# Kernel tuning notes

Hardware: AMD Instinct MI355X
Metric: run time of the kernel (lower is better)

Reference implementation:

```python
import jax, jax.numpy as jnp
from jax import lax
import numpy as np

NF, G, K = 64, 8, 3
B, H, W = 4, 128, 128
KK = K * K
CG = NF // G  # channels per deformable group


def setup_inputs() -> dict:
    key = jax.random.key(0)
    ks = jax.random.split(key, 8)
    f32 = jnp.float32
    s = 0.05  # small init so predicted offsets stay in a realistic range
    return {
        'nbr_fea_l': jax.random.normal(ks[0], (B, NF, H, W), f32),
        'ref_fea_l': jax.random.normal(ks[1], (B, NF, H, W), f32),
        'w_off1': jax.random.normal(ks[2], (NF, 2 * NF, K, K), f32) * s,
        'b_off1': jax.random.normal(ks[3], (NF,), f32) * s,
        'w_om': jax.random.normal(ks[4], (3 * G * KK, NF, K, K), f32) * s,
        'b_om': jax.random.normal(ks[5], (3 * G * KK,), f32) * s,
        'w_dcn': jax.random.normal(ks[6], (NF, NF, K, K), f32) * s,
        'b_dcn': jax.random.normal(ks[7], (NF,), f32) * s,
    }


def _conv3(x, w, b):
    # 3x3, stride 1, pad 1, NCHW/OIHW
    y = lax.conv_general_dilated(x, w, (1, 1), ((1, 1), (1, 1)))
    return y + b[None, :, None, None]


def _lrelu(x):
    return jnp.where(x >= 0, x, 0.1 * x)


def _gather_one(xf, idx):
    # xf: [CG, H*W], idx: [KK, H, W] -> [CG, KK, H, W]
    return jnp.take(xf, idx, axis=1)


_gather = jax.vmap(jax.vmap(_gather_one))  # over B, G


def _bilinear(x_flat, py, px):
    # x_flat: [B,G,CG,H*W]; py/px: [B,G,KK,H,W] sample coords
    y0f = jnp.floor(py)
    x0f = jnp.floor(px)
    wy = py - y0f
    wx = px - x0f
    y0 = y0f.astype(jnp.int32)
    x0 = x0f.astype(jnp.int32)
    out = jnp.zeros(x_flat.shape[:3] + py.shape[2:], x_flat.dtype)
    corners = [(0, 0, (1 - wy) * (1 - wx)), (0, 1, (1 - wy) * wx),
               (1, 0, wy * (1 - wx)), (1, 1, wy * wx)]
    for dy, dx, wgt in corners:
        yy = y0 + dy
        xx = x0 + dx
        valid = ((yy >= 0) & (yy < H) & (xx >= 0) & (xx < W)).astype(x_flat.dtype)
        idx = jnp.clip(yy, 0, H - 1) * W + jnp.clip(xx, 0, W - 1)
        g = _gather(x_flat, idx)  # [B,G,CG,KK,H,W]
        out = out + g * (wgt * valid)[:, :, None]
    return out


def _forward(nbr, ref, w_off1, b_off1, w_om, b_om, w_dcn, b_dcn):
    # offset feature branch
    off_feat = _lrelu(_conv3(jnp.concatenate([nbr, ref], axis=1), w_off1, b_off1))
    om = _conv3(off_feat, w_om, b_om)  # [B, 3*G*KK, H, W]
    o1, o2, m = jnp.split(om, 3, axis=1)
    off_y = o1.reshape(B, G, KK, H, W)
    off_x = o2.reshape(B, G, KK, H, W)
    mask = jax.nn.sigmoid(m).reshape(B, G, KK, H, W)
    # kernel tap displacements (pad=1, dilation=1, stride=1)
    dy = (jnp.repeat(jnp.arange(K), K) - 1).astype(nbr.dtype)  # [KK]
    dx = (jnp.tile(jnp.arange(K), K) - 1).astype(nbr.dtype)
    hh = jnp.arange(H, dtype=nbr.dtype)
    ww = jnp.arange(W, dtype=nbr.dtype)
    py = hh[None, None, None, :, None] + dy[None, None, :, None, None] + off_y
    px = ww[None, None, None, None, :] + dx[None, None, :, None, None] + off_x
    x_flat = nbr.reshape(B, G, CG, H * W)
    sampled = _bilinear(x_flat, py, px)           # [B,G,CG,KK,H,W]
    sampled = sampled * mask[:, :, None]          # modulated (DCNv2)
    w = w_dcn.reshape(NF, G, CG, KK)
    out = jnp.einsum('bgckhw,ogck->bohw', sampled, w) + b_dcn[None, :, None, None]
    return _lrelu(out)


def reference(nbr_fea_l, ref_fea_l, w_off1, b_off1, w_om, b_om, w_dcn, b_dcn):
    return _forward(nbr_fea_l, ref_fea_l, w_off1, b_off1, w_om, b_om, w_dcn, b_dcn)
```

## Files before the change

kernel.cpp:

```cpp
#include <hip/hip_runtime.h>
#include <hip/hip_bf16.h>
#include <hip/hip_fp16.h>
#include <cmath>

#define NF 64
#define GRP 8
#define CG 8
#define KK 9
#define HH 128
#define WWID 128
#define BB 4
#define HWSZ (HH * WWID)
#define C_OM 216
#define OMS 292
#define DPS 72

typedef __attribute__((ext_vector_type(8))) short bf16x8;
typedef __attribute__((ext_vector_type(8))) _Float16 f16x8;
typedef __attribute__((ext_vector_type(4))) float f32x4;

__device__ inline unsigned short f2bf(float f) {
    union { float f; unsigned u; } x; x.f = f;
    unsigned r = x.u + 0x7fff + ((x.u >> 16) & 1);
    return (unsigned short)(r >> 16);
}

__global__ __launch_bounds__(256) void prep_kernel(
    const float* __restrict__ nbr, const float* __restrict__ ref,
    const float* __restrict__ w1, const float* __restrict__ wom,
    const float* __restrict__ wdcn,
    unsigned short* __restrict__ out, unsigned short* __restrict__ gm,
    unsigned short* __restrict__ wf1, unsigned short* __restrict__ wf2,
    unsigned short* __restrict__ wdf)
{
    __shared__ unsigned short lds[64 * 136];
    __shared__ __half lds_h[64 * 72];
    const int tid = threadIdx.x;

    if (blockIdx.x < 1024) {
        const int blk = blockIdx.x;
        const int b = blk >> 8, rem = blk & 255, y = rem >> 1, x0 = (rem & 1) * 64;
        const size_t rowoff = (size_t)y * WWID + x0;

#pragma unroll
        for (int it = 0; it < 8; ++it) {
            int idx = it * 256 + tid;
            int c = idx >> 4, p4 = idx & 15;
            const float* src = (c < NF) ? (nbr + (size_t)(b * NF + c) * HWSZ)
                                        : (ref + (size_t)(b * NF + c - NF) * HWSZ);
            const float4 v = *(const float4*)(src + rowoff + p4 * 4);
            const float vv[4] = {v.x, v.y, v.z, v.w};
#pragma unroll
            for (int k = 0; k < 4; ++k) {
                const int p = p4 * 4 + k;
                lds[p * 136 + c] = f2bf(vv[k]);
                if (c < 64) lds_h[p * 72 + c] = __float2half(vv[k]);
            }
        }
        __syncthreads();
        const int p = tid >> 2, c0 = (tid & 3) * 32;
        unsigned short* dst = out + ((size_t)b * HWSZ + rowoff + p) * 128 + c0;
#pragma unroll
        for (int i = 0; i < 8; ++i)
            *(int2*)(dst + i * 4) = *(const int2*)&lds[p * 136 + c0 + i * 4];
        if (c0 < 64) {
#pragma unroll
            for (int gi = 0; gi < 4; ++gi) {
                const int g = (c0 >> 3) + gi;
                *(int4*)(gm + (((size_t)(b * 8 + g)) * HWSZ + rowoff + p) * 8) =
                    *(const int4*)&lds_h[p * 72 + g * 8];
            }
        }
        return;
    }

    int idx = (blockIdx.x - 1024) * 256 + tid;
    if (idx < 73728) {
        int j = idx & 7, lane = (idx >> 3) & 63, t = idx >> 9;
        int mt = t % 4, kt = t / 4;
        int c0 = (kt / 9) * 32, tap = kt - (kt / 9) * 9;
        int cout = mt * 16 + (lane & 15);
        int cin = c0 + ((lane >> 4) * 8) + j;
        wf1[idx] = f2bf(w1[((size_t)cout * 128 + cin) * KK + tap]);
        return;
    }
    idx -= 73728;
    if (idx < 129024) {
        int j = idx & 7, lane = (idx >> 3) & 63, t = idx >> 9;
        int mt = t % 14, kt = t / 14;
        int c0 = (kt / 9) * 32, tap = kt - (kt / 9) * 9;
        int cout = mt * 16 + (lane & 15);
        int cin = c0 + ((lane >> 4) * 8) + j;
        float v = (cout < C_OM) ? wom[((size_t)cout * 64 + cin) * KK + tap] : 0.f;
        wf2[idx] = f2bf(v);
        return;
    }
    idx -= 129024;
    if (idx < 36864) {
        int j = idx & 7, lane = (idx >> 3) & 63, t = idx >> 9;
        int mt = t & 3, s = t >> 2;
        int cout = mt * 16 + (lane & 15);
        int kglob = s * 32 + (lane >> 4) * 8 + j;
        int gk = kglob >> 3, c = kglob & 7;
        int g = gk / 9, kt = gk - g * 9;
        const __half hv = __float2half(wdcn[((size_t)cout * NF + g * 8 + c) * 9 + kt]);
        wdf[idx] = *(const unsigned short*)&hv;
    }
}

__global__ __launch_bounds__(256) void conv1_kernel(
    const unsigned short* __restrict__ in,
    const unsigned short* __restrict__ wf,
    const float* __restrict__ bias,
    unsigned short* __restrict__ dst)
{
    __shared__ unsigned short st[3 * 66 * DPS];

    const int tid = threadIdx.x;
    const int lane = tid & 63;
    const int wv = tid >> 6;
    const int ng = blockIdx.x;
    const int b = ng >> 8, rem = ng & 255;
    const int y = rem >> 1, x0 = (rem & 1) * 64;
    const int ln = lane & 15, kb = lane >> 4;

    f32x4 acc[4];
#pragma unroll
    for (int nt = 0; nt < 4; ++nt) acc[nt] = f32x4{0.f, 0.f, 0.f, 0.f};

    for (int ch0 = 0; ch0 < 128; ch0 += 64) {
        __syncthreads();
        for (int i = tid; i < 3 * 66 * 8; i += 256) {
            const int j = i & 7, t = i >> 3;
            const int px = t % 66, r = t / 66;
            const int yy = y + r - 1, xx = x0 + px - 1;
            int4 v = {0, 0, 0, 0};
            if ((unsigned)yy < (unsigned)HH && (unsigned)xx < (unsigned)WWID)
                v = *(const int4*)(in + ((size_t)b * HWSZ + yy * WWID + xx) * 128
                                      + ch0 + j * 8);
            *(int4*)&st[(r * 66 + px) * DPS + j * 8] = v;
        }
        __syncthreads();

        const int base_kt = (ch0 / 32) * 9;
        bf16x8 afA, afB;
        afA = *(const bf16x8*)(wf + (((size_t)base_kt * 4 + wv) * 64 + lane) * 8);

#pragma unroll
        for (int step = 0; step < 18; ++step) {
            const int cc = (step / 9) * 32;
            const int tap = step % 9;
            const int ky = tap / 3, kx = tap % 3;

            if (step < 17) {
                const int kt1 = base_kt + step + 1;
                bf16x8* alt = (step & 1) ? &afA : &afB;
                *alt = *(const bf16x8*)(wf + (((size_t)kt1 * 4 + wv) * 64 + lane) * 8);
            }

            bf16x8 bfrag[4];
#pragma unroll
            for (int nt = 0; nt < 4; ++nt) {
                const int px = nt * 16 + ln + kx;
                bfrag[nt] = *(const bf16x8*)&st[(ky * 66 + px) * DPS + cc + kb * 8];
            }

            const bf16x8 cur = (step & 1) ? afB : afA;
#pragma unroll
            for (int nt = 0; nt < 4; ++nt)
                acc[nt] = __builtin_amdgcn_mfma_f32_16x16x32_bf16(
                    cur, bfrag[nt], acc[nt], 0, 0, 0);
        }
    }

    const int cout = wv * 16 + kb * 4;
    const float b0 = bias[cout], b1 = bias[cout + 1];
    const float b2 = bias[cout + 2], b3 = bias[cout + 3];
#pragma unroll
    for (int nt = 0; nt < 4; ++nt) {
        const int px = x0 + nt * 16 + ln;
        const size_t pix = (size_t)b * HWSZ + (size_t)y * WWID + px;
        f32x4 v = acc[nt];
        v[0] += b0; v[1] += b1; v[2] += b2; v[3] += b3;
#pragma unroll
        for (int r = 0; r < 4; ++r) v[r] = (v[r] >= 0.f) ? v[r] : 0.1f * v[r];
        int2 pk;
        pk.x = (int)f2bf(v[0]) | ((int)f2bf(v[1]) << 16);
        pk.y = (int)f2bf(v[2]) | ((int)f2bf(v[3]) << 16);
        *(int2*)(dst + pix * 64 + cout) = pk;
    }
}

__global__ __launch_bounds__(512, 4) void dcn_fused_kernel(
    const unsigned short* __restrict__ off_f,
    const unsigned short* __restrict__ gm,
    const unsigned short* __restrict__ wf2,
    const float* __restrict__ bom,
    const unsigned short* __restrict__ wdf,
    const float* __restrict__ bdcn,
    float* __restrict__ out)
{
    __shared__ unsigned short smem[128 * OMS];

    const int raw = blockIdx.x;
    const int bid = (raw & 7) * 64 + (raw >> 3);
    const int b = bid >> 7;
    const int y = bid & 127;

    const int tid = threadIdx.x;
    const int lane = tid & 63;
    const int wv = tid >> 6;
    const int ln = lane & 15, kb = lane >> 4;

    for (int i = tid; i < 3 * 130 * 8; i += 512) {
        const int j = i & 7, t = i >> 3;
        const int px = t % 130, r = t / 130;
        const int yy = y + r - 1, xx = px - 1;
        int4 v = {0, 0, 0, 0};
        if ((unsigned)yy < (unsigned)HH && (unsigned)xx < (unsigned)WWID)
            v = *(const int4*)(off_f + ((size_t)b * HWSZ + yy * WWID + xx) * 64 + j * 8);
        *(int4*)&smem[(r * 130 + px) * DPS + j * 8] = v;
    }
    __syncthreads();

    f32x4 acc1[2][8];
#pragma unroll
    for (int i = 0; i < 2; ++i)
#pragma unroll
        for (int j = 0; j < 8; ++j) acc1[i][j] = f32x4{0.f, 0.f, 0.f, 0.f};

    {
        bf16x8 afA[2], afB[2];
#pragma unroll
        for (int i = 0; i < 2; ++i) {
            const int mt = wv + 8 * i;
            afA[i] = (mt < 14)
                ? ((const bf16x8*)wf2)[(size_t)mt * 64 + lane]
                : bf16x8{};
        }

#pragma unroll
        for (int step = 0; step < 18; ++step) {
            const int cc = (step / 9) * 32;
            const int tap = step % 9;
            const int ky = tap / 3, kx = tap % 3;

            if (step < 17) {
                const int kt1 = step + 1;
                bf16x8* alt = (step & 1) ? afA : afB;
#pragma unroll
                for (int i = 0; i < 2; ++i) {
                    const int mt = wv + 8 * i;
                    alt[i] = (mt < 14)
                        ? ((const bf16x8*)wf2)[(size_t)kt1 * 14 * 64 + (size_t)mt * 64 + lane]
                        : bf16x8{};
                }
            }

            bf16x8 bfrag[8];
#pragma unroll
            for (int nt = 0; nt < 8; ++nt) {
                const int px = nt * 16 + ln + kx;
                bfrag[nt] = *(const bf16x8*)&smem[(ky * 130 + px) * DPS + cc + kb * 8];
            }

            const bf16x8* cur = (step & 1) ? afB : afA;
#pragma unroll
            for (int i = 0; i < 2; ++i) {
                const int mt = wv + 8 * i;
                if (mt < 14) {
#pragma unroll
                    for (int nt = 0; nt < 8; ++nt)
                        acc1[i][nt] = __builtin_amdgcn_mfma_f32_16x16x32_bf16(
                            cur[i], bfrag[nt], acc1[i][nt], 0, 0, 0);
                }
            }
        }
    }
    __syncthreads();

    __half* smh = (__half*)smem;
#pragma unroll
    for (int i = 0; i < 2; ++i) {
        const int mt = wv + 8 * i;
        if (mt >= 14) continue;
        const int cb = mt * 16 + kb * 4;
#pragma unroll
        for (int nt = 0; nt < 8; ++nt) {
            const int px = nt * 16 + ln;
#pragma unroll
            for (int r = 0; r < 4; ++r) {
                const int c = cb + r;
                if (c < C_OM) {
                    const int field = (c >= 144) ? 2 : ((c >= 72) ? 1 : 0);
                    const int gk = c - field * 72;
                    float v = acc1[i][nt][r] + bom[c];
                    if (field == 2) v = 1.f / (1.f + __expf(-v));
                    smh[px * OMS + gk * 4 + field] = __float2half(v);
                }
            }
        }
    }
    __syncthreads();

    const int pxl = wv * 16 + ln;
    const int x = pxl;

    f32x4 acc[4];
#pragma unroll
    for (int mt = 0; mt < 4; ++mt) acc[mt] = f32x4{0.f, 0.f, 0.f, 0.f};

    const unsigned short* gmb = gm + (size_t)b * 8 * HWSZ * 8;

#pragma unroll
    for (int ch = 0; ch < 3; ++ch) {
        short4 q[6];
#pragma unroll
        for (int i = 0; i < 6; ++i) {
            const int gk = (ch * 6 + i) * 4 + kb;
            q[i] = *(const short4*)&smh[pxl * OMS + gk * 4];
        }

#pragma unroll
        for (int i = 0; i < 6; ++i) {
            const int s = ch * 6 + i;
            const int gk = s * 4 + kb;
            const int g = gk / 9;
            const int kt = gk - g * 9;

            const float oy = __half2float(((const __half*)&q[i])[0]);
            const float ox = __half2float(((const __half*)&q[i])[1]);
            const float mv = __half2float(((const __half*)&q[i])[2]);

            const float pyf = (float)(y + kt / 3 - 1) + oy;
            const float pxf = (float)(x + kt % 3 - 1) + ox;
            const float fy = floorf(pyf), fx = floorf(pxf);
            const float wy = pyf - fy, wx = pxf - fx;
            const int iy = (int)fy, ix = (int)fx;

            float w00 = (1.f - wy) * (1.f - wx);
            float w01 = (1.f - wy) * wx;
            float w10 = wy * (1.f - wx);
            float w11 = wy * wx;

            const bool vy0 = (iy >= 0) && (iy < HH);
            const bool vy1 = (iy + 1 >= 0) && (iy + 1 < HH);
            const bool vx0 = (ix >= 0) && (ix < WWID);
            const bool vx1 = (ix + 1 >= 0) && (ix + 1 < WWID);
            w00 *= (vy0 && vx0) ? mv : 0.f;
            w01 *= (vy0 && vx1) ? mv : 0.f;
            w10 *= (vy1 && vx0) ? mv : 0.f;
            w11 *= (vy1 && vx1) ? mv : 0.f;

            const int y0c = min(max(iy, 0), HH - 1);
            const int y1c = min(max(iy + 1, 0), HH - 1);
            const int x0c = min(max(ix, 0), WWID - 1);
            const int x1c = min(max(ix + 1, 0), WWID - 1);
            const int sel = x1c - x0c;

            const float wl0 = w00 + (sel ? 0.f : w01);
            const float wh0 = sel ? w01 : 0.f;
            const float wl1 = w10 + (sel ? 0.f : w11);
            const float wh1 = sel ? w11 : 0.f;

            const unsigned short* pgm = gmb + (size_t)g * HWSZ * 8;
            const size_t rec0 = (size_t)(y0c * WWID + x0c) * 8;
            const size_t rec1 = (size_t)(y1c * WWID + x0c) * 8;
            int4 L0 = *(const int4*)(pgm + rec0);
            int4 H0 = *(const int4*)(pgm + rec0 + 8);
            int4 L1 = *(const int4*)(pgm + rec1);
            int4 H1 = *(const int4*)(pgm + rec1 + 8);

            const __half2 wl0h = __float2half2_rn(wl0);
            const __half2 wh0h = __float2half2_rn(wh0);
            const __half2 wl1h = __float2half2_rn(wl1);
            const __half2 wh1h = __float2half2_rn(wh1);
            const __half2* l0 = (const __half2*)&L0;
            const __half2* h0 = (const __half2*)&H0;
            const __half2* l1 = (const __half2*)&L1;
            const __half2* h1 = (const __half2*)&H1;
            __half2 bp0 = __hfma2(l0[0], wl0h, __hfma2(h0[0], wh0h,
                          __hfma2(l1[0], wl1h, __hmul2(h1[0], wh1h))));
            __half2 bp1 = __hfma2(l0[1], wl0h, __hfma2(h0[1], wh0h,
                          __hfma2(l1[1], wl1h, __hmul2(h1[1], wh1h))));
            __half2 bp2 = __hfma2(l0[2], wl0h, __hfma2(h0[2], wh0h,
                          __hfma2(l1[2], wl1h, __hmul2(h1[2], wh1h))));
            __half2 bp3 = __hfma2(l0[3], wl0h, __hfma2(h0[3], wh0h,
                          __hfma2(l1[3], wl1h, __hmul2(h1[3], wh1h))));
            __half2 bpv[4] = {bp0, bp1, bp2, bp3};
            const f16x8 bfrag = *(const f16x8*)bpv;

            const f16x8* af = (const f16x8*)wdf + ((size_t)s * 4) * 64 + lane;
#pragma unroll
            for (int mt = 0; mt < 4; ++mt)
                acc[mt] = __builtin_amdgcn_mfma_f32_16x16x32_f16(
                    af[(size_t)mt * 64], bfrag, acc[mt], 0, 0, 0);
        }
    }

#pragma unroll
    for (int mt = 0; mt < 4; ++mt) {
#pragma unroll
        for (int r = 0; r < 4; ++r) {
            const int cout = mt * 16 + kb * 4 + r;
            float v = acc[mt][r] + bdcn[cout];
            v = (v >= 0.f) ? v : 0.1f * v;
            out[((size_t)(b * NF + cout)) * HWSZ + (size_t)y * WWID + x] = v;
        }
    }
}

extern "C" void kernel_launch(void* const* d_in, const int* in_sizes, int n_in,
                              void* d_out, int out_size, void* d_ws, size_t ws_size,
                              hipStream_t stream)
{
    const float* nbr  = (const float*)d_in[0];
    const float* ref  = (const float*)d_in[1];
    const float* w1   = (const float*)d_in[2];
    const float* b1   = (const float*)d_in[3];
    const float* wom  = (const float*)d_in[4];
    const float* bom  = (const float*)d_in[5];
    const float* wdcn = (const float*)d_in[6];
    const float* bdcn = (const float*)d_in[7];
    float* out = (float*)d_out;

    const size_t NH_B  = (size_t)BB * HWSZ * 128 * 2;
    const size_t OFF_B = (size_t)BB * HWSZ * 64 * 2;
    const size_t GM_B  = (size_t)BB * HWSZ * 64 * 2 + 64;
    const size_t WF1_B = 36 * 4 * 512 * 2;
    const size_t WF2_B = 18 * 14 * 512 * 2;

    char* ws = (char*)d_ws;
    unsigned short* nhwcin = (unsigned short*)ws;
    unsigned short* off_f  = (unsigned short*)(ws + NH_B);
    unsigned short* gm     = (unsigned short*)(ws + NH_B + OFF_B);
    unsigned short* wf1    = (unsigned short*)(ws + NH_B + OFF_B + GM_B);
    unsigned short* wf2    = wf1 + WF1_B / 2;
    unsigned short* wdf    = wf2 + WF2_B / 2;

    prep_kernel<<<1024 + 936, 256, 0, stream>>>(
        nbr, ref, w1, wom, wdcn, nhwcin, gm, wf1, wf2, wdf);

    conv1_kernel<<<1024, 256, 0, stream>>>(nhwcin, wf1, b1, off_f);

    dcn_fused_kernel<<<512, 512, 0, stream>>>(
        off_f, gm, wf2, bom, wdf, bdcn, out);
}
```

Measured before the change: 88.38 us.

## Prefetch second channel half into registers during conv1 compute; swizzle block order

The conv1 kernel now loads the second 64-channel half of the input halo into registers before running the MFMA loop on the first half, then writes those registers to shared memory afterward. The global-load latency of the second stage is meant to overlap with the first stage's compute. The block index is also remapped so that consecutive blocks are spread across batches and rows. The cost is 7 int4 registers per thread, which may reduce occupancy.

Measured after the change: 87.00 us (median of 2 runs). No clear change (-1.6%).

```diff
diff --git a/kernel.cpp b/kernel.cpp
--- a/kernel.cpp
+++ b/kernel.cpp
@@ -119,7 +119,8 @@
     const int tid = threadIdx.x;
     const int lane = tid & 63;
     const int wv = tid >> 6;
-    const int ng = blockIdx.x;
+    const int raw = blockIdx.x;
+    const int ng = (raw & 7) * 128 + (raw >> 3);
     const int b = ng >> 8, rem = ng & 255;
     const int y = rem >> 1, x0 = (rem & 1) * 64;
     const int ln = lane & 15, kb = lane >> 4;
@@ -128,24 +129,37 @@
 #pragma unroll
     for (int nt = 0; nt < 4; ++nt) acc[nt] = f32x4{0.f, 0.f, 0.f, 0.f};
 
-    for (int ch0 = 0; ch0 < 128; ch0 += 64) {
-        __syncthreads();
-        for (int i = tid; i < 3 * 66 * 8; i += 256) {
+    const unsigned short* inb = in + (size_t)b * HWSZ * 128;
+
+    for (int i = tid; i < 3 * 66 * 8; i += 256) {
+        const int j = i & 7, t = i >> 3;
+        const int px = t % 66, r = t / 66;
+        const int yy = y + r - 1, xx = x0 + px - 1;
+        int4 v = {0, 0, 0, 0};
+        if ((unsigned)yy < (unsigned)HH && (unsigned)xx < (unsigned)WWID)
+            v = *(const int4*)(inb + ((size_t)yy * WWID + xx) * 128 + j * 8);
+        *(int4*)&st[(r * 66 + px) * DPS + j * 8] = v;
+    }
+    __syncthreads();
+
+    int4 rg[7];
+#pragma unroll
+    for (int k = 0; k < 7; ++k) {
+        const int i = tid + k * 256;
+        int4 v = {0, 0, 0, 0};
+        if (i < 3 * 66 * 8) {
             const int j = i & 7, t = i >> 3;
             const int px = t % 66, r = t / 66;
             const int yy = y + r - 1, xx = x0 + px - 1;
-            int4 v = {0, 0, 0, 0};
             if ((unsigned)yy < (unsigned)HH && (unsigned)xx < (unsigned)WWID)
-                v = *(const int4*)(in + ((size_t)b * HWSZ + yy * WWID + xx) * 128
-                                      + ch0 + j * 8);
-            *(int4*)&st[(r * 66 + px) * DPS + j * 8] = v;
-        }
-        __syncthreads();
-
-        const int base_kt = (ch0 / 32) * 9;
+                v = *(const int4*)(inb + ((size_t)yy * WWID + xx) * 128 + 64 + j * 8);
+        }
+        rg[k] = v;
+    }
+
+    auto compute = [&](int base_kt) {
         bf16x8 afA, afB;
         afA = *(const bf16x8*)(wf + (((size_t)base_kt * 4 + wv) * 64 + lane) * 8);
-
 #pragma unroll
         for (int step = 0; step < 18; ++step) {
             const int cc = (step / 9) * 32;
@@ -171,7 +185,23 @@
                 acc[nt] = __builtin_amdgcn_mfma_f32_16x16x32_bf16(
                     cur, bfrag[nt], acc[nt], 0, 0, 0);
         }
-    }
+    };
+
+    compute(0);
+    __syncthreads();
+
+#pragma unroll
+    for (int k = 0; k < 7; ++k) {
+        const int i = tid + k * 256;
+        if (i < 3 * 66 * 8) {
+            const int j = i & 7, t = i >> 3;
+            const int px = t % 66, r = t / 66;
+            *(int4*)&st[(r * 66 + px) * DPS + j * 8] = rg[k];
+        }
+    }
+    __syncthreads();
+
+    compute(18);
 
     const int cout = wv * 16 + kb * 4;
     const float b0 = bias[cout], b1 = bias[cout + 1];
```
